# Optimization experiments

Measured on AMD Instinct MI355X. Metric: run time of the kernel, lower is better.

## Reference

```python
import jax, jax.numpy as jnp
import numpy as np

B, S, F, H = 2, 2048, 2048, 16
DH = F // H  # head_dim = 128
ROPE_BASE = 10000.0


def apply_rope(x, offset):
    # x: [B, S, H, Dh]; rotate-half RoPE per head with positions offset..offset+S-1
    d = x.shape[-1]
    pos = jnp.arange(x.shape[1], dtype=jnp.float32) + offset          # [S]
    inv_freq = 1.0 / (ROPE_BASE ** (jnp.arange(0, d, 2, dtype=jnp.float32) / d))  # [Dh/2]
    ang = pos[:, None] * inv_freq[None, :]                             # [S, Dh/2]
    cos = jnp.cos(ang)[None, :, None, :].astype(x.dtype)               # [1,S,1,Dh/2]
    sin = jnp.sin(ang)[None, :, None, :].astype(x.dtype)
    x1, x2 = x[..., : d // 2], x[..., d // 2 :]
    return jnp.concatenate([x1 * cos - x2 * sin, x1 * sin + x2 * cos], axis=-1)


def setup_inputs() -> dict:
    key = jax.random.key(0)
    k0, k1, k2, k3 = jax.random.split(key, 4)
    lecun = (1.0 / F) ** 0.5
    in_q = jax.random.normal(k0, (B, S, F), dtype=jnp.float32)
    Wq = jax.random.normal(k1, (F, H, DH), dtype=jnp.float32) * lecun
    Wk = jax.random.normal(k2, (F, H, DH), dtype=jnp.float32) * lecun
    Wv = jax.random.normal(k3, (F, H, DH), dtype=jnp.float32) * lecun
    bq = jnp.zeros((H, DH), dtype=jnp.float32)
    bk = jnp.zeros((H, DH), dtype=jnp.float32)
    bv = jnp.zeros((H, DH), dtype=jnp.float32)
    mask = jnp.tril(jnp.ones((S, S), dtype=bool))[None, None, :, :]  # causal [1,1,S,S]
    return {"in_q": in_q, "Wq": Wq, "bq": bq, "Wk": Wk, "bk": bk,
            "Wv": Wv, "bv": bv, "mask": mask, "offset": 0}


def reference(in_q, Wq, bq, Wk, bk, Wv, bv, mask, offset):
    # QKV projections: LinearGeneral [B,S,F] x [F,H,Dh] -> [B,S,H,Dh]
    q = jnp.einsum("bsf,fhd->bshd", in_q, Wq) + bq
    k = jnp.einsum("bsf,fhd->bshd", in_q, Wk) + bk
    v = jnp.einsum("bsf,fhd->bshd", in_q, Wv) + bv
    # RoPE on q and k (merge/split-head reshape in original is a no-op on values)
    q = apply_rope(q, offset)
    k = apply_rope(k, offset)
    # dot-product attention
    scale = 1.0 / jnp.sqrt(jnp.asarray(DH, dtype=q.dtype))
    scores = jnp.einsum("bqhd,bkhd->bhqk", q, k) * scale   # [B,H,Sq,Skv]
    scores = jnp.where(mask, scores, jnp.finfo(scores.dtype).min)
    weights = jax.nn.softmax(scores, axis=-1)
    out = jnp.einsum("bhqk,bkhd->bqhd", weights, v)        # [B,S,H,Dh]
    return out.reshape(out.shape[0], out.shape[1], H * DH)  # merge heads
```

## Files before the change

### kernel.cpp

```cpp
#include <hip/hip_runtime.h>
#include <hip/hip_bf16.h>
#include <stdint.h>

#define NB 2
#define NS 2048
#define NFE 2048
#define NH 16
#define NDH 128

#define QSCALE (0.08838834764831845f * 1.4426950408889634f)

typedef __attribute__((ext_vector_type(4))) float f32x4;
typedef __attribute__((ext_vector_type(8))) __bf16 bf16x8;

__device__ __forceinline__ uint16_t f2bf(float f) {
  uint32_t u = __builtin_bit_cast(uint32_t, f);
  return (uint16_t)((u + 0x7fffu + ((u >> 16) & 1u)) >> 16);
}

__device__ __forceinline__ void gload_lds16(const void* g, void* l) {
  __builtin_amdgcn_global_load_lds((const __attribute__((address_space(1))) void*)g,
                                   (__attribute__((address_space(3))) void*)l,
                                   16, 0, 0);
}

#define MFMA16(a, b, c) __builtin_amdgcn_mfma_f32_16x16x32_bf16(a, b, c, 0, 0, 0)

__global__ void k_convert(const float* __restrict__ x, uint16_t* __restrict__ y) {
  int i = (blockIdx.x * 256 + threadIdx.x) * 4;
  float4 v = *(const float4*)(x + i);
  ushort4 o;
  o.x = f2bf(v.x); o.y = f2bf(v.y); o.z = f2bf(v.z); o.w = f2bf(v.w);
  *(ushort4*)(y + i) = o;
}

__global__ void k_wt(const float* __restrict__ Wq, const float* __restrict__ Wk,
                     const float* __restrict__ Wv, uint16_t* __restrict__ Wt) {
  int which = blockIdx.z;
  const float* Wsrc = (which == 0) ? Wq : ((which == 1) ? Wk : Wv);
  int k0 = blockIdx.x * 64, n0 = blockIdx.y * 64;
  __shared__ uint16_t tile[64][65];
  int t = threadIdx.x;
#pragma unroll
  for (int it = 0; it < 4; ++it) {
    int vec = t + it * 256;
    int r = vec >> 4, c4 = vec & 15;
    float4 v = *(const float4*)&Wsrc[(size_t)(k0 + r) * NFE + n0 + c4 * 4];
    tile[r][c4 * 4 + 0] = f2bf(v.x);
    tile[r][c4 * 4 + 1] = f2bf(v.y);
    tile[r][c4 * 4 + 2] = f2bf(v.z);
    tile[r][c4 * 4 + 3] = f2bf(v.w);
  }
  __syncthreads();
#pragma unroll
  for (int it = 0; it < 4; ++it) {
    int vec = t + it * 256;
    int r = vec >> 4, c4 = vec & 15;
    ushort4 o;
    o.x = tile[c4 * 4 + 0][r];
    o.y = tile[c4 * 4 + 1][r];
    o.z = tile[c4 * 4 + 2][r];
    o.w = tile[c4 * 4 + 3][r];
    *(ushort4*)&Wt[(size_t)which * NFE * NFE + (size_t)(n0 + r) * NFE + k0 + c4 * 4] = o;
  }
}

__global__ void k_rope_tab(float* __restrict__ cosT, float* __restrict__ sinT,
                           const int* __restrict__ offp) {
  int tid = blockIdx.x * 256 + threadIdx.x;
  int s = tid >> 6, i = tid & 63;
  float off = (float)offp[0];
  float inv = expf(-((float)i / 64.0f) * logf(10000.0f));
  float ang = ((float)s + off) * inv;
  cosT[tid] = cosf(ang);
  sinT[tid] = sinf(ang);
}

__global__ __launch_bounds__(256, 2) void k_gemm_qkv(
    const uint16_t* __restrict__ A, const uint16_t* __restrict__ Wt,
    const float* __restrict__ bq, const float* __restrict__ bk, const float* __restrict__ bv,
    const float* __restrict__ cosT, const float* __restrict__ sinT,
    uint16_t* __restrict__ qws, uint16_t* __restrict__ kws, uint16_t* __restrict__ vws) {
  __shared__ alignas(16) uint16_t Asm[128 * 64];
  __shared__ alignas(16) uint16_t Bsm[128 * 64];
  int mt = blockIdx.x;
  int nt = blockIdx.y;
  int which = nt >> 4, h = nt & 15;
  const uint16_t* Bsrc = Wt + (size_t)which * NFE * NFE + (size_t)h * NDH * NFE;
  const uint16_t* Arow = A + (size_t)mt * 128 * NFE;
  int t = threadIdx.x, w = t >> 6, l = t & 63;
  int g = l >> 4, c = l & 15;

  f32x4 acc[2][8];
#pragma unroll
  for (int m = 0; m < 2; ++m)
#pragma unroll
    for (int n = 0; n < 8; ++n) acc[m][n] = (f32x4){0.f, 0.f, 0.f, 0.f};

  for (int kt = 0; kt < NFE / 64; ++kt) {
    int k0 = kt * 64;
#pragma unroll
    for (int cc = 0; cc < 4; ++cc) {
      int flat = cc * 256 + t;
      int row = flat >> 3, sub = flat & 7;
      int scol = ((sub ^ (row & 7)) << 3) + k0;
      gload_lds16(&Arow[(size_t)row * NFE + scol], (char*)Asm + flat * 16);
    }
#pragma unroll
    for (int cc = 0; cc < 4; ++cc) {
      int flat = cc * 256 + t;
      int row = flat >> 3, sub = flat & 7;
      int scol = ((sub ^ (row & 7)) << 3) + k0;
      gload_lds16(&Bsrc[(size_t)row * NFE + scol], (char*)Bsm + flat * 16);
    }
    __syncthreads();
#pragma unroll
    for (int ks = 0; ks < 2; ++ks) {
      bf16x8 af[2];
#pragma unroll
      for (int m = 0; m < 2; ++m) {
        int row = w * 32 + m * 16 + c;
        int kb = ((ks * 32 + g * 8) * 2) ^ ((row & 7) << 4);
        af[m] = *(const bf16x8*)((const char*)Asm + row * 128 + kb);
      }
#pragma unroll
      for (int nf = 0; nf < 8; ++nf) {
        int row = nf * 16 + c;
        int kb = ((ks * 32 + g * 8) * 2) ^ ((row & 7) << 4);
        bf16x8 bfr = *(const bf16x8*)((const char*)Bsm + row * 128 + kb);
        acc[0][nf] = MFMA16(af[0], bfr, acc[0][nf]);
        acc[1][nf] = MFMA16(af[1], bfr, acc[1][nf]);
      }
    }
    __syncthreads();
  }

  const float* bias = (which == 0) ? bq : ((which == 1) ? bk : bv);
  uint16_t* outp = (which == 0) ? qws : ((which == 1) ? kws : vws);
  float scl = (which == 0) ? QSCALE : 1.0f;
  int mbase = mt * 128 + w * 32;
  if (which < 2) {
#pragma unroll
    for (int m = 0; m < 2; ++m)
#pragma unroll
      for (int nf = 0; nf < 4; ++nf) {
        int i = nf * 16 + c;
        float b1 = bias[h * NDH + i], b2 = bias[h * NDH + 64 + i];
#pragma unroll
        for (int j = 0; j < 4; ++j) {
          int r = mbase + m * 16 + g * 4 + j;
          int bb = r >> 11, s = r & (NS - 1);
          float cs = cosT[(s << 6) + i], sn = sinT[(s << 6) + i];
          float x1 = acc[m][nf][j] + b1;
          float x2 = acc[m][nf + 4][j] + b2;
          uint16_t* op = outp + ((size_t)(bb * NH + h) * NS + s) * NDH;
          op[i] = f2bf((x1 * cs - x2 * sn) * scl);
          op[64 + i] = f2bf((x1 * sn + x2 * cs) * scl);
        }
      }
  } else {
#pragma unroll
    for (int m = 0; m < 2; ++m)
#pragma unroll
      for (int nf = 0; nf < 8; ++nf) {
        int d = nf * 16 + c;
        float bv_ = bias[h * NDH + d];
#pragma unroll
        for (int j = 0; j < 4; ++j) {
          int r = mbase + m * 16 + g * 4 + j;
          int bb = r >> 11, s = r & (NS - 1);
          outp[((size_t)(bb * NH + h) * NS + s) * NDH + d] = f2bf(acc[m][nf][j] + bv_);
        }
      }
  }
}

__global__ void k_vt(const uint16_t* __restrict__ v, uint16_t* __restrict__ vt) {
  int bh = blockIdx.z;
  int s0 = blockIdx.x * 64, d0 = blockIdx.y * 64;
  __shared__ uint16_t tile[64][65];
  int t = threadIdx.x;
#pragma unroll
  for (int it = 0; it < 4; ++it) {
    int vec = t + it * 256;
    int r = vec >> 4, c4 = vec & 15;
    ushort4 x = *(const ushort4*)&v[((size_t)bh * NS + s0 + r) * NDH + d0 + c4 * 4];
    tile[r][c4 * 4 + 0] = x.x;
    tile[r][c4 * 4 + 1] = x.y;
    tile[r][c4 * 4 + 2] = x.z;
    tile[r][c4 * 4 + 3] = x.w;
  }
  __syncthreads();
#pragma unroll
  for (int it = 0; it < 4; ++it) {
    int vec = t + it * 256;
    int r = vec >> 4, c4 = vec & 15;
    ushort4 o;
    o.x = tile[c4 * 4 + 0][r];
    o.y = tile[c4 * 4 + 1][r];
    o.z = tile[c4 * 4 + 2][r];
    o.w = tile[c4 * 4 + 3][r];
    *(ushort4*)&vt[((size_t)bh * NDH + d0 + r) * NS + s0 + c4 * 4] = o;
  }
}

__global__ __launch_bounds__(256, 4) void k_attn(
    const uint16_t* __restrict__ qws, const uint16_t* __restrict__ kws,
    const uint16_t* __restrict__ vtws, float* __restrict__ out) {
  __shared__ alignas(16) uint16_t Ksm[64 * 128];
  __shared__ alignas(16) uint16_t Vsm[128 * 64];
  __shared__ alignas(16) uint16_t Psm[4][16 * 64];

  int bh = blockIdx.x;
  int t = threadIdx.x, w = t >> 6, l = t & 63;
  int g = l >> 4, c = l & 15;
  int bb = bh >> 4, h = bh & 15;

  const uint16_t* Qp = qws + (size_t)bh * NS * NDH;
  const uint16_t* Kp = kws + (size_t)bh * NS * NDH;
  const uint16_t* Vp = vtws + (size_t)bh * NDH * NS;

  for (int pass = 0; pass < 2; ++pass) {
    int y64 = pass ? (31 - blockIdx.y) : blockIdx.y;
    int q0 = y64 * 64;
    int r = q0 + w * 16 + c;

    bf16x8 qf[4];
#pragma unroll
    for (int kk = 0; kk < 4; ++kk)
      qf[kk] = *(const bf16x8*)&Qp[(size_t)r * NDH + kk * 32 + g * 8];

    f32x4 acc_o[8];
    float mreg = -1e30f, lreg = 0.f;
#pragma unroll
    for (int n = 0; n < 8; ++n) acc_o[n] = (f32x4){0.f, 0.f, 0.f, 0.f};

    int nkt = y64 + 1;
    for (int kt = 0; kt < nkt; ++kt) {
#pragma unroll
      for (int cc = 0; cc < 4; ++cc) {
        int flat = cc * 256 + t;
        int row = flat >> 4, sub = flat & 15;
        int scol = ((sub ^ (row & 7)) << 3);
        gload_lds16(&Kp[(size_t)(kt * 64 + row) * NDH + scol], (char*)Ksm + flat * 16);
      }
#pragma unroll
      for (int cc = 0; cc < 4; ++cc) {
        int flat = cc * 256 + t;
        int row = flat >> 3, sub = flat & 7;
        int scol = ((sub ^ (row & 7)) << 3);
        gload_lds16(&Vp[(size_t)row * NS + kt * 64 + scol], (char*)Vsm + flat * 16);
      }
      __syncthreads();

      f32x4 sacc[4];
#pragma unroll
      for (int nf = 0; nf < 4; ++nf) sacc[nf] = (f32x4){0.f, 0.f, 0.f, 0.f};
#pragma unroll
      for (int kk = 0; kk < 4; ++kk) {
#pragma unroll
        for (int nf = 0; nf < 4; ++nf) {
          int row = nf * 16 + c;
          int kb = ((kk * 32 + g * 8) * 2) ^ ((row & 7) << 4);
          bf16x8 kfr = *(const bf16x8*)((const char*)Ksm + row * 256 + kb);
          sacc[nf] = MFMA16(kfr, qf[kk], sacc[nf]);
        }
      }

      if (kt == y64) {
#pragma unroll
        for (int nf = 0; nf < 4; ++nf)
#pragma unroll
          for (int j = 0; j < 4; ++j) {
            int kv = kt * 64 + nf * 16 + g * 4 + j;
            if (kv > r) sacc[nf][j] = -1e30f;
          }
      }

      float mx = -1e30f;
#pragma unroll
      for (int nf = 0; nf < 4; ++nf)
        mx = fmaxf(mx, fmaxf(fmaxf(sacc[nf][0], sacc[nf][1]),
                             fmaxf(sacc[nf][2], sacc[nf][3])));
      mx = fmaxf(mx, __shfl_xor(mx, 16));
      mx = fmaxf(mx, __shfl_xor(mx, 32));

      float mnew = mreg;
      if (!__all(mx <= mreg + 8.0f)) {
        mnew = fmaxf(mreg, mx);
        float alpha = exp2f(mreg - mnew);
        mreg = mnew;
        lreg *= alpha;
#pragma unroll
        for (int j = 0; j < 4; ++j) {
          float aj = __shfl(alpha, (l & 48) + g * 4 + j);
#pragma unroll
          for (int nf = 0; nf < 8; ++nf) acc_o[nf][j] *= aj;
        }
      }

      float rs = 0.f;
#pragma unroll
      for (int nf = 0; nf < 4; ++nf)
#pragma unroll
        for (int j = 0; j < 4; ++j) {
          float p = exp2f(sacc[nf][j] - mnew);
          sacc[nf][j] = p;
          rs += p;
        }
      rs += __shfl_xor(rs, 16);
      rs += __shfl_xor(rs, 32);
      lreg += rs;

#pragma unroll
      for (int nf = 0; nf < 4; ++nf) {
        uint32_t pk0 = (uint32_t)f2bf(sacc[nf][0]) | ((uint32_t)f2bf(sacc[nf][1]) << 16);
        uint32_t pk1 = (uint32_t)f2bf(sacc[nf][2]) | ((uint32_t)f2bf(sacc[nf][3]) << 16);
        int colb = (nf * 16 + g * 4) * 2;
        char* base = (char*)Psm[w] + c * 128;
        *(uint32_t*)(base + (colb ^ ((c & 7) << 4))) = pk0;
        *(uint32_t*)(base + ((colb + 4) ^ ((c & 7) << 4))) = pk1;
      }

#pragma unroll
      for (int kk2 = 0; kk2 < 2; ++kk2) {
        int prow = c;
        int pkb = ((kk2 * 32 + g * 8) * 2) ^ ((prow & 7) << 4);
        bf16x8 pf = *(const bf16x8*)((const char*)Psm[w] + prow * 128 + pkb);
#pragma unroll
        for (int nf = 0; nf < 8; ++nf) {
          int row = nf * 16 + c;
          int kb = ((kk2 * 32 + g * 8) * 2) ^ ((row & 7) << 4);
          bf16x8 vf = *(const bf16x8*)((const char*)Vsm + row * 128 + kb);
          acc_o[nf] = MFMA16(pf, vf, acc_o[nf]);
        }
      }
      __syncthreads();
    }

#pragma unroll
    for (int j = 0; j < 4; ++j) {
      float lj = __shfl(lreg, (l & 48) + g * 4 + j);
      float inv = 1.0f / lj;
      int s = q0 + w * 16 + g * 4 + j;
      float* op = out + ((size_t)(bb * NS + s)) * NFE + h * NDH;
#pragma unroll
      for (int nf = 0; nf < 8; ++nf) op[nf * 16 + c] = acc_o[nf][j] * inv;
    }
  }
}

extern "C" void kernel_launch(void* const* d_in, const int* in_sizes, int n_in,
                              void* d_out, int out_size, void* d_ws, size_t ws_size,
                              hipStream_t stream) {
  const float* in_q = (const float*)d_in[0];
  const float* Wq = (const float*)d_in[1];
  const float* bq = (const float*)d_in[2];
  const float* Wk = (const float*)d_in[3];
  const float* bk = (const float*)d_in[4];
  const float* Wv = (const float*)d_in[5];
  const float* bv = (const float*)d_in[6];
  const int* offp = (const int*)d_in[8];
  float* out = (float*)d_out;

  char* ws = (char*)d_ws;
  const size_t SZ_AQ = (size_t)4096 * 2048 * 2;
  const size_t SZ_WT = (size_t)3 * 2048 * 2048 * 2;
  const size_t SZ_TAB = (size_t)2048 * 64 * 4;
  const size_t SZ_QKV = (size_t)32 * 2048 * 128 * 2;
  uint16_t* Aq = (uint16_t*)(ws);
  uint16_t* Wt = (uint16_t*)(ws + SZ_AQ);
  float* cosT = (float*)(ws + SZ_AQ + SZ_WT);
  float* sinT = (float*)(ws + SZ_AQ + SZ_WT + SZ_TAB);
  uint16_t* qws = (uint16_t*)(ws + SZ_AQ + SZ_WT + 2 * SZ_TAB);
  uint16_t* kws = (uint16_t*)(ws + SZ_AQ + SZ_WT + 2 * SZ_TAB + SZ_QKV);
  uint16_t* vws = (uint16_t*)(ws + SZ_AQ + SZ_WT + 2 * SZ_TAB + 2 * SZ_QKV);
  uint16_t* vtws = (uint16_t*)(ws + SZ_AQ + SZ_WT + 2 * SZ_TAB + 3 * SZ_QKV);

  k_convert<<<8192, 256, 0, stream>>>(in_q, Aq);
  k_wt<<<dim3(32, 32, 3), 256, 0, stream>>>(Wq, Wk, Wv, Wt);
  k_rope_tab<<<512, 256, 0, stream>>>(cosT, sinT, offp);
  k_gemm_qkv<<<dim3(32, 48), 256, 0, stream>>>(Aq, Wt, bq, bk, bv, cosT, sinT, qws, kws, vws);
  k_vt<<<dim3(32, 2, 32), 256, 0, stream>>>(vws, vtws);
  k_attn<<<dim3(32, 16), 256, 0, stream>>>(qws, kws, vtws, out);
}
```

Baseline: 210.2 us.

## Rewrite QKV GEMM as 256x256 double-buffered ping-pong pipelined kernel

The QKV projection GEMM moves from 128x128 tiles with single-buffered LDS and two barriers per k-step to 256x256 tiles on 512 threads. It double-buffers A and B in LDS and interleaves global-to-LDS prefetch with MFMA phases using explicit waitcnt, barriers and setprio scheduling. It also adds a 1D grid with a block-index swizzle for L2 locality. The aim is to hide memory latency and raise arithmetic intensity. The cost is 128KB of LDS and heavy register pressure, which may limit occupancy.

```diff
diff --git a/kernel.cpp b/kernel.cpp
--- a/kernel.cpp
+++ b/kernel.cpp
@@ -76,91 +76,156 @@
   sinT[tid] = sinf(ang);
 }
 
-__global__ __launch_bounds__(256, 2) void k_gemm_qkv(
+__global__ __launch_bounds__(512, 2) void k_gemm_qkv(
     const uint16_t* __restrict__ A, const uint16_t* __restrict__ Wt,
     const float* __restrict__ bq, const float* __restrict__ bk, const float* __restrict__ bv,
     const float* __restrict__ cosT, const float* __restrict__ sinT,
     uint16_t* __restrict__ qws, uint16_t* __restrict__ kws, uint16_t* __restrict__ vws) {
-  __shared__ alignas(16) uint16_t Asm[128 * 64];
-  __shared__ alignas(16) uint16_t Bsm[128 * 64];
-  int mt = blockIdx.x;
-  int nt = blockIdx.y;
-  int which = nt >> 4, h = nt & 15;
-  const uint16_t* Bsrc = Wt + (size_t)which * NFE * NFE + (size_t)h * NDH * NFE;
-  const uint16_t* Arow = A + (size_t)mt * 128 * NFE;
-  int t = threadIdx.x, w = t >> 6, l = t & 63;
+  __shared__ uint16_t SMEM[4][16384];
+
+  int bid = blockIdx.x;
+  int swzb = (bid & 7) * 48 + (bid >> 3);
+  int bx = swzb & 15, by = swzb >> 4;
+  int t = threadIdx.x, l = t & 63, w = t >> 6;
   int g = l >> 4, c = l & 15;
-
-  f32x4 acc[2][8];
-#pragma unroll
-  for (int m = 0; m < 2; ++m)
+  int wr = w >> 1, wc = w & 1;
+
+  int row0 = t >> 3;
+  int swz = ((t & 7) ^ (row0 & 7)) << 3;
+  const uint16_t* aTh = A + ((size_t)bx * 256 + row0) * NFE + swz;
+  const uint16_t* bTh = Wt + ((size_t)by * 256 + row0) * NFE + swz;
+
+#define STG(sbase, slot, h, kt)                                                   \
+  do {                                                                            \
+    const uint16_t* _s = (sbase) + (size_t)((h) * 128) * NFE + (size_t)(kt) * 64; \
+    char* _d = (char*)(&SMEM[slot][0]) + (h) * 16384 + t * 16;                    \
+    gload_lds16(_s, _d);                                                          \
+    gload_lds16(_s + (size_t)64 * NFE, _d + 8192);                                \
+  } while (0)
+
+#define LDA_(buf, mh)                                                             \
+  _Pragma("unroll") for (int mi = 0; mi < 2; ++mi)                                \
+  _Pragma("unroll") for (int kk = 0; kk < 2; ++kk) {                              \
+    int row = wr * 64 + ((mh) * 2 + mi) * 16 + c;                                 \
+    af[mi][kk] = *(const bf16x8*)((const char*)SMEM[(buf) * 2] + row * 128 +      \
+                                  (((kk * 4 + g) ^ (row & 7)) << 4));             \
+  }
+
+#define LDB_(buf, nh, BF)                                                         \
+  _Pragma("unroll") for (int ni = 0; ni < 4; ++ni)                                \
+  _Pragma("unroll") for (int kk = 0; kk < 2; ++kk) {                              \
+    int row = wc * 128 + ((nh) * 4 + ni) * 16 + c;                                \
+    BF[ni][kk] = *(const bf16x8*)((const char*)SMEM[(buf) * 2 + 1] + row * 128 +  \
+                                  (((kk * 4 + g) ^ (row & 7)) << 4));             \
+  }
+
+#define MM_(mh, nh, BF)                                                           \
+  _Pragma("unroll") for (int kk = 0; kk < 2; ++kk)                                \
+  _Pragma("unroll") for (int mi = 0; mi < 2; ++mi)                                \
+  _Pragma("unroll") for (int ni = 0; ni < 4; ++ni)                                \
+    acc[(mh) * 2 + mi][(nh) * 4 + ni] =                                           \
+        MFMA16(af[mi][kk], BF[ni][kk], acc[(mh) * 2 + mi][(nh) * 4 + ni]);
+
+#define BAR_MID()                                          \
+  do {                                                     \
+    __builtin_amdgcn_s_barrier();                          \
+    asm volatile("s_waitcnt lgkmcnt(0)" ::: "memory");     \
+    __builtin_amdgcn_sched_barrier(0);                     \
+    __builtin_amdgcn_s_setprio(1);                         \
+  } while (0)
+#define BAR_END()                                          \
+  do {                                                     \
+    __builtin_amdgcn_s_setprio(0);                         \
+    __builtin_amdgcn_s_barrier();                          \
+  } while (0)
+
+  f32x4 acc[4][8];
+#pragma unroll
+  for (int m = 0; m < 4; ++m)
 #pragma unroll
     for (int n = 0; n < 8; ++n) acc[m][n] = (f32x4){0.f, 0.f, 0.f, 0.f};
 
-  for (int kt = 0; kt < NFE / 64; ++kt) {
-    int k0 = kt * 64;
-#pragma unroll
-    for (int cc = 0; cc < 4; ++cc) {
-      int flat = cc * 256 + t;
-      int row = flat >> 3, sub = flat & 7;
-      int scol = ((sub ^ (row & 7)) << 3) + k0;
-      gload_lds16(&Arow[(size_t)row * NFE + scol], (char*)Asm + flat * 16);
-    }
-#pragma unroll
-    for (int cc = 0; cc < 4; ++cc) {
-      int flat = cc * 256 + t;
-      int row = flat >> 3, sub = flat & 7;
-      int scol = ((sub ^ (row & 7)) << 3) + k0;
-      gload_lds16(&Bsrc[(size_t)row * NFE + scol], (char*)Bsm + flat * 16);
-    }
-    __syncthreads();
-#pragma unroll
-    for (int ks = 0; ks < 2; ++ks) {
-      bf16x8 af[2];
-#pragma unroll
-      for (int m = 0; m < 2; ++m) {
-        int row = w * 32 + m * 16 + c;
-        int kb = ((ks * 32 + g * 8) * 2) ^ ((row & 7) << 4);
-        af[m] = *(const bf16x8*)((const char*)Asm + row * 128 + kb);
-      }
-#pragma unroll
-      for (int nf = 0; nf < 8; ++nf) {
-        int row = nf * 16 + c;
-        int kb = ((ks * 32 + g * 8) * 2) ^ ((row & 7) << 4);
-        bf16x8 bfr = *(const bf16x8*)((const char*)Bsm + row * 128 + kb);
-        acc[0][nf] = MFMA16(af[0], bfr, acc[0][nf]);
-        acc[1][nf] = MFMA16(af[1], bfr, acc[1][nf]);
-      }
-    }
-    __syncthreads();
-  }
-
+  bf16x8 af[2][2], bflo[4][2], bfhi[4][2];
+
+  STG(aTh, 0, 0, 0); STG(aTh, 0, 1, 0); STG(bTh, 1, 0, 0); STG(bTh, 1, 1, 0);
+  STG(aTh, 2, 0, 1); STG(aTh, 2, 1, 1); STG(bTh, 3, 0, 1); STG(bTh, 3, 1, 1);
+  asm volatile("s_waitcnt vmcnt(8)" ::: "memory");
+  __builtin_amdgcn_s_barrier();
+
+  for (int i = 0; i < 15; ++i) {
+    int t2 = 2 * i + 2, t3 = 2 * i + 3;
+    LDA_(0, 0); LDB_(0, 0, bflo);
+    BAR_MID(); MM_(0, 0, bflo); BAR_END();
+    LDB_(0, 1, bfhi);
+    BAR_MID(); MM_(0, 1, bfhi); BAR_END();
+    LDA_(0, 1);
+    STG(bTh, 1, 0, t2);
+    BAR_MID(); MM_(1, 1, bfhi); BAR_END();
+    STG(bTh, 1, 1, t2);
+    asm volatile("s_waitcnt vmcnt(4)" ::: "memory");
+    BAR_MID(); MM_(1, 0, bflo); BAR_END();
+    LDA_(1, 0); LDB_(1, 0, bflo);
+    STG(aTh, 0, 0, t2);
+    BAR_MID(); MM_(0, 0, bflo); BAR_END();
+    LDB_(1, 1, bfhi);
+    STG(aTh, 0, 1, t2);
+    BAR_MID(); MM_(0, 1, bfhi); BAR_END();
+    LDA_(1, 1);
+    STG(bTh, 3, 0, t3);
+    BAR_MID(); MM_(1, 1, bfhi); BAR_END();
+    STG(bTh, 3, 1, t3);
+    STG(aTh, 2, 0, t3);
+    STG(aTh, 2, 1, t3);
+    asm volatile("s_waitcnt vmcnt(8)" ::: "memory");
+    BAR_MID(); MM_(1, 0, bflo); BAR_END();
+  }
+
+  {
+    LDA_(0, 0); LDB_(0, 0, bflo);
+    BAR_MID(); MM_(0, 0, bflo); BAR_END();
+    LDB_(0, 1, bfhi);
+    BAR_MID(); MM_(0, 1, bfhi); BAR_END();
+    LDA_(0, 1);
+    BAR_MID(); MM_(1, 1, bfhi); BAR_END();
+    asm volatile("s_waitcnt vmcnt(0)" ::: "memory");
+    BAR_MID(); MM_(1, 0, bflo); BAR_END();
+    LDA_(1, 0); LDB_(1, 0, bflo);
+    BAR_MID(); MM_(0, 0, bflo); BAR_END();
+    LDB_(1, 1, bfhi);
+    BAR_MID(); MM_(0, 1, bfhi); BAR_END();
+    LDA_(1, 1);
+    BAR_MID(); MM_(1, 1, bfhi); BAR_END();
+    BAR_MID(); MM_(1, 0, bflo); BAR_END();
+  }
+
+  int ghead = by * 2 + wc;
+  int which = ghead >> 4, h = ghead & 15;
   const float* bias = (which == 0) ? bq : ((which == 1) ? bk : bv);
   uint16_t* outp = (which == 0) ? qws : ((which == 1) ? kws : vws);
   float scl = (which == 0) ? QSCALE : 1.0f;
-  int mbase = mt * 128 + w * 32;
+  int mbase = bx * 256 + wr * 64;
   if (which < 2) {
 #pragma unroll
-    for (int m = 0; m < 2; ++m)
+    for (int m = 0; m < 4; ++m)
 #pragma unroll
       for (int nf = 0; nf < 4; ++nf) {
-        int i = nf * 16 + c;
-        float b1 = bias[h * NDH + i], b2 = bias[h * NDH + 64 + i];
+        int i2 = nf * 16 + c;
+        float b1 = bias[h * NDH + i2], b2 = bias[h * NDH + 64 + i2];
 #pragma unroll
         for (int j = 0; j < 4; ++j) {
           int r = mbase + m * 16 + g * 4 + j;
           int bb = r >> 11, s = r & (NS - 1);
-          float cs = cosT[(s << 6) + i], sn = sinT[(s << 6) + i];
+          float cs = cosT[(s << 6) + i2], sn = sinT[(s << 6) + i2];
           float x1 = acc[m][nf][j] + b1;
           float x2 = acc[m][nf + 4][j] + b2;
           uint16_t* op = outp + ((size_t)(bb * NH + h) * NS + s) * NDH;
-          op[i] = f2bf((x1 * cs - x2 * sn) * scl);
-          op[64 + i] = f2bf((x1 * sn + x2 * cs) * scl);
+          op[i2] = f2bf((x1 * cs - x2 * sn) * scl);
+          op[64 + i2] = f2bf((x1 * sn + x2 * cs) * scl);
         }
       }
   } else {
 #pragma unroll
-    for (int m = 0; m < 2; ++m)
+    for (int m = 0; m < 4; ++m)
 #pragma unroll
       for (int nf = 0; nf < 8; ++nf) {
         int d = nf * 16 + c;
@@ -173,6 +238,12 @@
         }
       }
   }
+#undef STG
+#undef LDA_
+#undef LDB_
+#undef MM_
+#undef BAR_MID
+#undef BAR_END
 }
 
 __global__ void k_vt(const uint16_t* __restrict__ v, uint16_t* __restrict__ vt) {
@@ -380,7 +451,7 @@
   k_convert<<<8192, 256, 0, stream>>>(in_q, Aq);
   k_wt<<<dim3(32, 32, 3), 256, 0, stream>>>(Wq, Wk, Wv, Wt);
   k_rope_tab<<<512, 256, 0, stream>>>(cosT, sinT, offp);
-  k_gemm_qkv<<<dim3(32, 48), 256, 0, stream>>>(Aq, Wt, bq, bk, bv, cosT, sinT, qws, kws, vws);
+  k_gemm_qkv<<<384, 512, 0, stream>>>(Aq, Wt, bq, bk, bv, cosT, sinT, qws, kws, vws);
   k_vt<<<dim3(32, 2, 32), 256, 0, stream>>>(vws, vtws);
   k_attn<<<dim3(32, 16), 256, 0, stream>>>(qws, kws, vtws, out);
 }
```

New measurement: 227.9 us. 8.4% more time.
